# Performance work log

Measured on AMD Instinct MI355X. Metric: run time of the kernel, lower is better.

Reference implementation:

```python
import jax, jax.numpy as jnp
import numpy as np

B, S, D_IN, D_OUT = 4, 2048, 1024, 1024


def setup_inputs() -> dict:
    key = jax.random.key(0)
    k1, k2, k3, k4 = jax.random.split(key, 4)
    scale = 1.0 / np.sqrt(D_IN)
    return {
        "x": jax.random.normal(k1, (B, S, D_IN), dtype=jnp.float32),
        "W_q": jax.random.normal(k2, (D_IN, D_OUT), dtype=jnp.float32) * scale,
        "W_k": jax.random.normal(k3, (D_IN, D_OUT), dtype=jnp.float32) * scale,
        "W_v": jax.random.normal(k4, (D_IN, D_OUT), dtype=jnp.float32) * scale,
    }


def reference(x, W_q, W_k, W_v):
    # x: [B, S, D_IN]; weights stored as [D_IN, D_OUT] (transpose of torch Linear)
    q = x @ W_q  # [B, S, D_OUT]
    k = x @ W_k
    v = x @ W_v
    inv_sqrt_d = 1.0 / jnp.sqrt(jnp.asarray(k.shape[-1], dtype=q.dtype))
    scores = jnp.einsum("bqd,bkd->bqk", q, k) * inv_sqrt_d  # [B, S, S]
    n = x.shape[1]
    causal_mask = jnp.triu(jnp.ones((n, n), dtype=bool), k=1)  # True above diagonal
    scores = jnp.where(causal_mask, -jnp.inf, scores)
    attn = jax.nn.softmax(scores, axis=-1)  # dropout p=0.0 -> identity
    return jnp.einsum("bqk,bkd->bqd", attn, v)  # [B, S, D_OUT]
```

## Files before the change

kernel.cpp:

```cpp
#include <hip/hip_runtime.h>
#include <hip/hip_bf16.h>
#include <stdint.h>

typedef __bf16 bf16;
typedef bf16 bf16x8 __attribute__((ext_vector_type(8)));
typedef float f32x4 __attribute__((ext_vector_type(4)));

#define NB   4
#define SS   2048
#define DI   1024
#define DOUT 1024

__device__ __forceinline__ void gload_lds16(const void* g, void* l) {
  __builtin_amdgcn_global_load_lds(
      (const __attribute__((address_space(1))) void*)g,
      (__attribute__((address_space(3))) void*)l, 16, 0, 0);
}

#define BARX  { __builtin_amdgcn_s_barrier(); __builtin_amdgcn_sched_barrier(0); }
#define VMW12 asm volatile("s_waitcnt vmcnt(12)" ::: "memory")
#define VMW8  asm volatile("s_waitcnt vmcnt(8)"  ::: "memory")
#define VMW6  asm volatile("s_waitcnt vmcnt(6)"  ::: "memory")
#define VMW4  asm volatile("s_waitcnt vmcnt(4)"  ::: "memory")
#define VMW0  asm volatile("s_waitcnt vmcnt(0)"  ::: "memory")

__device__ __forceinline__ void r5_loop3(
    const bf16* __restrict__ Ag, int lda,
    const bf16* __restrict__ Bg, int ldb,
    int nt, char* lds, f32x4 (&acc)[8][4])
{
  const int tid = threadIdx.x, lane = tid & 63, w = tid >> 6;
  const int g    = (tid & 3) ^ ((tid >> 3) & 3);
  const int srow = tid >> 2;
  const int l15  = lane & 15, lg = lane >> 4;
  const int aoff = l15 * 64 + ((lg ^ ((l15 >> 1) & 3)) << 4);

  auto STG = [&](int t, int p) {
    char* Ab = lds + p * 24576;
    char* Bb = lds + p * 24576 + 8192;
#pragma unroll
    for (int i = 0; i < 2; ++i)
      gload_lds16(Ag + (size_t)(i * 64 + srow) * lda + t * 32 + g * 8,
                  Ab + i * 4096 + tid * 16);
#pragma unroll
    for (int i = 0; i < 4; ++i)
      gload_lds16(Bg + (size_t)(i * 64 + srow) * ldb + t * 32 + g * 8,
                  Bb + i * 4096 + tid * 16);
  };

  auto CMP = [&](int p) {
    const char* Ab = lds + p * 24576;
    const char* Bb = lds + p * 24576 + 8192 + w * 4096;
    bf16x8 a[8], bq[4];
#pragma unroll
    for (int am = 0; am < 8; ++am) a[am] = *(const bf16x8*)(Ab + am * 1024 + aoff);
#pragma unroll
    for (int fn = 0; fn < 4; ++fn) bq[fn] = *(const bf16x8*)(Bb + fn * 1024 + aoff);
    __builtin_amdgcn_s_setprio(1);
#pragma unroll
    for (int am = 0; am < 8; ++am)
#pragma unroll
      for (int fn = 0; fn < 4; ++fn)
        acc[am][fn] = __builtin_amdgcn_mfma_f32_16x16x32_bf16(
            a[am], bq[fn], acc[am][fn], 0, 0, 0);
    __builtin_amdgcn_s_setprio(0);
  };

  STG(0, 0);
  STG(1, 1);
  int pw = 2, pr = 0;
  for (int t = 0; t < nt - 2; ++t) {
    STG(t + 2, pw);
    VMW12;
    BARX;
    CMP(pr);
    BARX;
    pw = (pw == 2) ? 0 : pw + 1;
    pr = (pr == 2) ? 0 : pr + 1;
  }
  VMW6; BARX; CMP(pr); BARX;
  pr = (pr == 2) ? 0 : pr + 1;
  VMW0; BARX; CMP(pr);
}

__device__ __forceinline__ void r5h_loop3(
    const bf16* __restrict__ Ag, int lda,
    const bf16* __restrict__ Bg, int ldb,
    int nt, char* lds, f32x4 (&acc)[4][4])
{
  const int tid = threadIdx.x, lane = tid & 63, wid = tid >> 6;
  const int wr = wid >> 1, wc = wid & 1;
  const int g    = (tid & 3) ^ ((tid >> 3) & 3);
  const int srow = tid >> 2;
  const int l15  = lane & 15, lg = lane >> 4;
  const int aoff = l15 * 64 + ((lg ^ ((l15 >> 1) & 3)) << 4);

  auto STG = [&](int t, int p) {
    char* Ab = lds + p * 16384;
    char* Bb = lds + p * 16384 + 8192;
#pragma unroll
    for (int i = 0; i < 2; ++i) {
      gload_lds16(Ag + (size_t)(i * 64 + srow) * lda + t * 32 + g * 8,
                  Ab + i * 4096 + tid * 16);
      gload_lds16(Bg + (size_t)(i * 64 + srow) * ldb + t * 32 + g * 8,
                  Bb + i * 4096 + tid * 16);
    }
  };

  auto CMP = [&](int p) {
    const char* Ab = lds + p * 16384 + wr * 4096;
    const char* Bb = lds + p * 16384 + 8192 + wc * 4096;
    bf16x8 a[4], bq[4];
#pragma unroll
    for (int fm = 0; fm < 4; ++fm) a[fm] = *(const bf16x8*)(Ab + fm * 1024 + aoff);
#pragma unroll
    for (int fn = 0; fn < 4; ++fn) bq[fn] = *(const bf16x8*)(Bb + fn * 1024 + aoff);
    __builtin_amdgcn_s_setprio(1);
#pragma unroll
    for (int fm = 0; fm < 4; ++fm)
#pragma unroll
      for (int fn = 0; fn < 4; ++fn)
        acc[fm][fn] = __builtin_amdgcn_mfma_f32_16x16x32_bf16(
            a[fm], bq[fn], acc[fm][fn], 0, 0, 0);
    __builtin_amdgcn_s_setprio(0);
  };

  STG(0, 0);
  STG(1, 1);
  int pw = 2, pr = 0;
  for (int t = 0; t < nt - 2; ++t) {
    STG(t + 2, pw);
    VMW8;
    BARX;
    CMP(pr);
    BARX;
    pw = (pw == 2) ? 0 : pw + 1;
    pr = (pr == 2) ? 0 : pr + 1;
  }
  VMW4; BARX; CMP(pr); BARX;
  pr = (pr == 2) ? 0 : pr + 1;
  VMW0; BARX; CMP(pr);
}

__device__ __forceinline__ void acc_zero4(f32x4 (&acc)[4][4]) {
#pragma unroll
  for (int i = 0; i < 4; ++i)
#pragma unroll
    for (int j = 0; j < 4; ++j)
      acc[i][j] = (f32x4){0.f, 0.f, 0.f, 0.f};
}

__global__ __launch_bounds__(256) void k_cast_wt(const float* __restrict__ Wq,
                                                 const float* __restrict__ Wk,
                                                 const float* __restrict__ Wv,
                                                 bf16* __restrict__ WSq,
                                                 bf16* __restrict__ WSk,
                                                 bf16* __restrict__ WTv) {
  __shared__ float t[32][33];
  const int w = blockIdx.z;
  const int k0 = blockIdx.y * 32, c0 = blockIdx.x * 32;
  const int tx = threadIdx.x, ty = threadIdx.y;
  if (w < 2) {
    const float* W = w ? Wk : Wq;
    bf16* WS = w ? WSk : WSq;
#pragma unroll
    for (int i = 0; i < 4; ++i) {
      const size_t idx = (size_t)(k0 + ty + 8 * i) * DI + c0 + tx;
      WS[idx] = (bf16)W[idx];
    }
  } else {
#pragma unroll
    for (int i = 0; i < 4; ++i)
      t[ty + 8 * i][tx] = Wv[(size_t)(k0 + ty + 8 * i) * DI + c0 + tx];
    __syncthreads();
#pragma unroll
    for (int i = 0; i < 4; ++i)
      WTv[(size_t)(c0 + ty + 8 * i) * DI + k0 + tx] = (bf16)t[tx][ty + 8 * i];
  }
}

__global__ __launch_bounds__(256) void k_castx_mt(const float* __restrict__ x,
                                                  bf16* __restrict__ xb,
                                                  const bf16* __restrict__ WSk,
                                                  const bf16* __restrict__ WSq,
                                                  bf16* __restrict__ MT) {
  __shared__ __align__(16) char lds[49152];
  const int bid = blockIdx.x;
  if (bid < 64) {
    const int m0 = (bid >> 3) * 128, n0 = (bid & 7) * 128;
    f32x4 acc[4][4];
    acc_zero4(acc);
    r5h_loop3(WSk + (size_t)m0 * 1024, 1024, WSq + (size_t)n0 * 1024, 1024,
              32, lds, acc);
    const int lane = threadIdx.x & 63, wid = threadIdx.x >> 6;
    const int wr = wid >> 1, wc = wid & 1;
    const int r4 = (lane >> 4) * 4, cn = lane & 15;
#pragma unroll
    for (int fm = 0; fm < 4; ++fm)
#pragma unroll
      for (int fn = 0; fn < 4; ++fn) {
        const int row = m0 + wr * 64 + fm * 16 + r4;
        const int col = n0 + wc * 64 + fn * 16 + cn;
#pragma unroll
        for (int rr = 0; rr < 4; ++rr)
          MT[(size_t)(row + rr) * 1024 + col] = (bf16)acc[fm][fn][rr];
      }
  } else {
    const size_t i = ((size_t)(bid - 64) * 256 + threadIdx.x) * 8;
    const float4 a = *(const float4*)(x + i);
    const float4 c = *(const float4*)(x + i + 4);
    bf16x8 v;
    v[0] = (bf16)a.x; v[1] = (bf16)a.y; v[2] = (bf16)a.z; v[3] = (bf16)a.w;
    v[4] = (bf16)c.x; v[5] = (bf16)c.y; v[6] = (bf16)c.z; v[7] = (bf16)c.w;
    *(bf16x8*)(xb + i) = v;
  }
}

__global__ __launch_bounds__(256, 2) void k_tv(const bf16* __restrict__ X,
                                               const bf16* __restrict__ MT,
                                               const bf16* __restrict__ WTv,
                                               bf16* __restrict__ T,
                                               bf16* __restrict__ VT) {
  __shared__ __align__(16) char lds[73728];
  const int bid  = blockIdx.x;
  const int wgid = (bid & 7) * 64 + (bid >> 3);
  const int m0 = (wgid >> 3) * 128;
  const int n0 = (wgid & 7) * 256;

  const bf16* Bg = (n0 < 1024) ? MT + (size_t)n0 * 1024
                               : WTv + (size_t)(n0 - 1024) * 1024;

  f32x4 acc[8][4];
#pragma unroll
  for (int i = 0; i < 8; ++i)
#pragma unroll
    for (int j = 0; j < 4; ++j)
      acc[i][j] = (f32x4){0.f, 0.f, 0.f, 0.f};

  r5_loop3(X + (size_t)m0 * 1024, 1024, Bg, 1024, 32, lds, acc);

  const int lane = threadIdx.x & 63, w = threadIdx.x >> 6;
  const int r4 = (lane >> 4) * 4;
  const int cn = lane & 15;
  if (n0 < 1024) {
#pragma unroll
    for (int am = 0; am < 8; ++am) {
      const int row = m0 + am * 16 + r4;
#pragma unroll
      for (int fn = 0; fn < 4; ++fn) {
        const int n = n0 + w * 64 + fn * 16 + cn;
        const size_t base = (size_t)row * 1024 + n;
#pragma unroll
        for (int r = 0; r < 4; ++r)
          T[base + (size_t)r * 1024] = (bf16)acc[am][fn][r];
      }
    }
  } else {
    const int b_ = m0 >> 11;
    const int sb = m0 & 2047;
#pragma unroll
    for (int am = 0; am < 8; ++am)
#pragma unroll
      for (int fn = 0; fn < 4; ++fn) {
        const int d  = (n0 - 1024) + w * 64 + fn * 16 + cn;
        const int s0 = sb + am * 16 + r4;
        ushort4 pk;
        pk.x = __builtin_bit_cast(unsigned short, (bf16)acc[am][fn][0]);
        pk.y = __builtin_bit_cast(unsigned short, (bf16)acc[am][fn][1]);
        pk.z = __builtin_bit_cast(unsigned short, (bf16)acc[am][fn][2]);
        pk.w = __builtin_bit_cast(unsigned short, (bf16)acc[am][fn][3]);
        *(ushort4*)(VT + ((size_t)b_ * DOUT + d) * SS + s0) = pk;
      }
  }
}

__global__ __launch_bounds__(256, 3) void k_gemm_qk(const bf16* __restrict__ T,
                                                    const bf16* __restrict__ XB,
                                                    bf16* __restrict__ E,
                                                    float* __restrict__ RS) {
  __shared__ __align__(16) char lds[49152];
  const int wfl = blockIdx.x;
  const int b = wfl / 136;
  int r = wfl % 136;
  int i = 0;
  for (;;) { const int cnt = i + 1; if (r < cnt) break; r -= cnt; ++i; }
  const int m0 = i * 128, n0 = r * 128;

  f32x4 acc[4][4];
  acc_zero4(acc);
  r5h_loop3(T  + ((size_t)b * SS + m0) * 1024, 1024,
            XB + ((size_t)b * SS + n0) * 1024, 1024, 32, lds, acc);

  bf16* Eb = E + (size_t)b * SS * SS;
  float* RSb = RS + (size_t)b * SS;
  const float scale = 0.03125f;
  const int lane = threadIdx.x & 63, wid = threadIdx.x >> 6;
  const int wr = wid >> 1, wc = wid & 1;
  const int r4 = (lane >> 4) * 4, cn = lane & 15;

  float rsum[4][4];
#pragma unroll
  for (int fm = 0; fm < 4; ++fm)
#pragma unroll
    for (int rr = 0; rr < 4; ++rr) rsum[fm][rr] = 0.f;

#pragma unroll
  for (int fm = 0; fm < 4; ++fm)
#pragma unroll
    for (int fn = 0; fn < 4; ++fn) {
      const int n = n0 + wc * 64 + fn * 16 + cn;
      const int rowb = m0 + wr * 64 + fm * 16 + r4;
      const size_t bofs = (size_t)rowb * SS + n;
#pragma unroll
      for (int rr = 0; rr < 4; ++rr) {
        const float e = (n <= rowb + rr) ? __expf(acc[fm][fn][rr] * scale) : 0.f;
        Eb[bofs + (size_t)rr * SS] = (bf16)e;
        rsum[fm][rr] += e;
      }
    }

#pragma unroll
  for (int fm = 0; fm < 4; ++fm)
#pragma unroll
    for (int rr = 0; rr < 4; ++rr) {
      float s = rsum[fm][rr];
      s += __shfl_xor(s, 1);
      s += __shfl_xor(s, 2);
      s += __shfl_xor(s, 4);
      s += __shfl_xor(s, 8);
      if (cn == 0)
        atomicAdd(&RSb[m0 + wr * 64 + fm * 16 + r4 + rr], s);
    }
}

__global__ __launch_bounds__(256, 3) void k_gemm_pv(const bf16* __restrict__ P,
                                                    const bf16* __restrict__ VT,
                                                    const float* __restrict__ RS,
                                                    float* __restrict__ Out) {
  __shared__ __align__(16) char lds[49152];
  const int wfl = blockIdx.x;
  const int h = wfl >> 8;
  const int r = wfl & 255;
  const int b = r >> 6;
  const int t = r & 63;
  const int ip = t >> 3;
  const int j = t & 7;
  const int i = h ? (15 - ip) : ip;
  const int m0 = i * 128, n0 = j * 128;
  const int nt = 4 * (i + 1);

  f32x4 acc[4][4];
  acc_zero4(acc);
  r5h_loop3(P  + (size_t)b * SS * SS   + (size_t)m0 * SS, SS,
            VT + (size_t)b * DOUT * SS + (size_t)n0 * SS, SS,
            nt, lds, acc);

  float* Ob = Out + (size_t)b * SS * DOUT;
  const float* RSb = RS + (size_t)b * SS;
  const int lane = threadIdx.x & 63, wid = threadIdx.x >> 6;
  const int wr = wid >> 1, wc = wid & 1;
  const int r4 = (lane >> 4) * 4, cn = lane & 15;
#pragma unroll
  for (int fm = 0; fm < 4; ++fm) {
    const int rowb = m0 + wr * 64 + fm * 16 + r4;
    const float4 rs4 = *(const float4*)(RSb + rowb);
    float inv[4];
    inv[0] = 1.0f / rs4.x; inv[1] = 1.0f / rs4.y;
    inv[2] = 1.0f / rs4.z; inv[3] = 1.0f / rs4.w;
#pragma unroll
    for (int fn = 0; fn < 4; ++fn) {
      const int n = n0 + wc * 64 + fn * 16 + cn;
      const size_t bofs = (size_t)rowb * DOUT + n;
#pragma unroll
      for (int rr = 0; rr < 4; ++rr)
        Ob[bofs + (size_t)rr * DOUT] = acc[fm][fn][rr] * inv[rr];
    }
  }
}

extern "C" void kernel_launch(void* const* d_in, const int* in_sizes, int n_in,
                              void* d_out, int out_size, void* d_ws, size_t ws_size,
                              hipStream_t stream) {
  const float* x  = (const float*)d_in[0];
  const float* Wq = (const float*)d_in[1];
  const float* Wk = (const float*)d_in[2];
  const float* Wv = (const float*)d_in[3];
  float* out = (float*)d_out;
  char* ws = (char*)d_ws;

  bf16*  T   = (bf16*)(ws);
  bf16*  VT  = (bf16*)(ws + ((size_t)16 << 20));
  bf16*  E   = (bf16*)(ws + ((size_t)32 << 20));
  bf16*  XB  = (bf16*)(ws + ((size_t)64 << 20));
  bf16*  WSq = (bf16*)(ws + ((size_t)80 << 20));
  bf16*  WSk = (bf16*)(ws + ((size_t)82 << 20));
  bf16*  WTv = (bf16*)(ws + ((size_t)84 << 20));
  bf16*  MT  = (bf16*)(ws + ((size_t)86 << 20));
  float* RS  = (float*)(ws + ((size_t)88 << 20));

  hipMemsetAsync(RS, 0, (size_t)NB * SS * sizeof(float), stream);
  k_cast_wt<<<dim3(32, 32, 3), dim3(32, 8), 0, stream>>>(Wq, Wk, Wv, WSq, WSk, WTv);
  k_castx_mt<<<4160, 256, 0, stream>>>(x, XB, WSk, WSq, MT);
  k_tv<<<512, 256, 0, stream>>>(XB, MT, WTv, T, VT);
  k_gemm_qk<<<544, 256, 0, stream>>>(T, XB, E, RS);
  k_gemm_pv<<<512, 256, 0, stream>>>(E, VT, RS, out);
}
```

Baseline: 144.2 us.

## Split-K the Wk·Wqᵀ product with fp32 atomics and fuse weight casts

The 1024x1024 Wk·Wq^T product was computed by only 64 blocks over the full K. It is now split eight ways along K into 512 blocks that read the fp32 weights directly, convert them to bf16 in LDS, and atomically add their partials into an fp32 buffer. A separate small kernel then converts that buffer to bf16. This removes the separate bf16 weight-cast pass for Wq/Wk and exposes more parallelism on a stage that was latency bound. The cost is atomic traffic, a larger memset (which also zeroes RS through the contiguous layout), one extra launch, and a simpler unpipelined inner loop.

```diff
diff --git a/kernel.cpp b/kernel.cpp
--- a/kernel.cpp
+++ b/kernel.cpp
@@ -23,6 +23,13 @@
 #define VMW6  asm volatile("s_waitcnt vmcnt(6)"  ::: "memory")
 #define VMW4  asm volatile("s_waitcnt vmcnt(4)"  ::: "memory")
 #define VMW0  asm volatile("s_waitcnt vmcnt(0)"  ::: "memory")
+
+__device__ __forceinline__ bf16x8 cvt8(float4 a, float4 b) {
+  bf16x8 v;
+  v[0] = (bf16)a.x; v[1] = (bf16)a.y; v[2] = (bf16)a.z; v[3] = (bf16)a.w;
+  v[4] = (bf16)b.x; v[5] = (bf16)b.y; v[6] = (bf16)b.z; v[7] = (bf16)b.w;
+  return v;
+}
 
 __device__ __forceinline__ void r5_loop3(
     const bf16* __restrict__ Ag, int lda,
@@ -150,25 +157,81 @@
       acc[i][j] = (f32x4){0.f, 0.f, 0.f, 0.f};
 }
 
-__global__ __launch_bounds__(256) void k_cast_wt(const float* __restrict__ Wq,
-                                                 const float* __restrict__ Wk,
-                                                 const float* __restrict__ Wv,
-                                                 bf16* __restrict__ WSq,
-                                                 bf16* __restrict__ WSk,
-                                                 bf16* __restrict__ WTv) {
-  __shared__ float t[32][33];
-  const int w = blockIdx.z;
-  const int k0 = blockIdx.y * 32, c0 = blockIdx.x * 32;
-  const int tx = threadIdx.x, ty = threadIdx.y;
-  if (w < 2) {
-    const float* W = w ? Wk : Wq;
-    bf16* WS = w ? WSk : WSq;
-#pragma unroll
-    for (int i = 0; i < 4; ++i) {
-      const size_t idx = (size_t)(k0 + ty + 8 * i) * DI + c0 + tx;
-      WS[idx] = (bf16)W[idx];
-    }
+__global__ __launch_bounds__(256) void k_prep1(const float* __restrict__ x,
+                                               bf16* __restrict__ xb,
+                                               const float* __restrict__ Wq,
+                                               const float* __restrict__ Wk,
+                                               const float* __restrict__ Wv,
+                                               bf16* __restrict__ WTv,
+                                               float* __restrict__ MTf) {
+  __shared__ __align__(16) char lds[16384];
+  const int bid = blockIdx.x;
+  const int tid = threadIdx.x;
+
+  if (bid < 512) {
+    const int tile = bid >> 3, s = bid & 7;
+    const int m0 = (tile >> 3) * 128, n0 = (tile & 7) * 128;
+    const int k0 = s * 128;
+    const int lane = tid & 63, wid = tid >> 6;
+    const int wr = wid >> 1, wc = wid & 1;
+    const int g    = (tid & 3) ^ ((tid >> 3) & 3);
+    const int srow = tid >> 2;
+    const int l15  = lane & 15, lg = lane >> 4;
+    const int aoff = l15 * 64 + ((lg ^ ((l15 >> 1) & 3)) << 4);
+
+    f32x4 acc[4][4];
+    acc_zero4(acc);
+
+    for (int t = 0; t < 4; ++t) {
+#pragma unroll
+      for (int i = 0; i < 2; ++i) {
+        const float* ap = Wk + (size_t)(m0 + i * 64 + srow) * DI + k0 + t * 32 + g * 8;
+        const float* bp = Wq + (size_t)(n0 + i * 64 + srow) * DI + k0 + t * 32 + g * 8;
+        const float4 a0 = *(const float4*)ap, a1 = *(const float4*)(ap + 4);
+        const float4 b0 = *(const float4*)bp, b1 = *(const float4*)(bp + 4);
+        *(bf16x8*)(lds + i * 4096 + tid * 16)        = cvt8(a0, a1);
+        *(bf16x8*)(lds + 8192 + i * 4096 + tid * 16) = cvt8(b0, b1);
+      }
+      __syncthreads();
+      {
+        const char* Ab = lds + wr * 4096;
+        const char* Bb = lds + 8192 + wc * 4096;
+        bf16x8 a[4], bq[4];
+#pragma unroll
+        for (int fm = 0; fm < 4; ++fm) a[fm] = *(const bf16x8*)(Ab + fm * 1024 + aoff);
+#pragma unroll
+        for (int fn = 0; fn < 4; ++fn) bq[fn] = *(const bf16x8*)(Bb + fn * 1024 + aoff);
+#pragma unroll
+        for (int fm = 0; fm < 4; ++fm)
+#pragma unroll
+          for (int fn = 0; fn < 4; ++fn)
+            acc[fm][fn] = __builtin_amdgcn_mfma_f32_16x16x32_bf16(
+                a[fm], bq[fn], acc[fm][fn], 0, 0, 0);
+      }
+      __syncthreads();
+    }
+
+    const int r4 = (lane >> 4) * 4, cn = lane & 15;
+#pragma unroll
+    for (int fm = 0; fm < 4; ++fm)
+#pragma unroll
+      for (int fn = 0; fn < 4; ++fn) {
+        const int rowb = m0 + wr * 64 + fm * 16 + r4;
+        const int col  = n0 + wc * 64 + fn * 16 + cn;
+#pragma unroll
+        for (int rr = 0; rr < 4; ++rr)
+          atomicAdd(&MTf[(size_t)(rowb + rr) * 1024 + col], acc[fm][fn][rr]);
+      }
+  } else if (bid < 4608) {
+    const size_t i = ((size_t)(bid - 512) * 256 + tid) * 8;
+    const float4 a = *(const float4*)(x + i);
+    const float4 c = *(const float4*)(x + i + 4);
+    *(bf16x8*)(xb + i) = cvt8(a, c);
   } else {
+    float (*t)[33] = (float (*)[33])lds;
+    const int tt = bid - 4608;
+    const int c0 = (tt & 31) * 32, k0 = (tt >> 5) * 32;
+    const int tx = tid & 31, ty = tid >> 5;
 #pragma unroll
     for (int i = 0; i < 4; ++i)
       t[ty + 8 * i][tx] = Wv[(size_t)(k0 + ty + 8 * i) * DI + c0 + tx];
@@ -179,41 +242,12 @@
   }
 }
 
-__global__ __launch_bounds__(256) void k_castx_mt(const float* __restrict__ x,
-                                                  bf16* __restrict__ xb,
-                                                  const bf16* __restrict__ WSk,
-                                                  const bf16* __restrict__ WSq,
-                                                  bf16* __restrict__ MT) {
-  __shared__ __align__(16) char lds[49152];
-  const int bid = blockIdx.x;
-  if (bid < 64) {
-    const int m0 = (bid >> 3) * 128, n0 = (bid & 7) * 128;
-    f32x4 acc[4][4];
-    acc_zero4(acc);
-    r5h_loop3(WSk + (size_t)m0 * 1024, 1024, WSq + (size_t)n0 * 1024, 1024,
-              32, lds, acc);
-    const int lane = threadIdx.x & 63, wid = threadIdx.x >> 6;
-    const int wr = wid >> 1, wc = wid & 1;
-    const int r4 = (lane >> 4) * 4, cn = lane & 15;
-#pragma unroll
-    for (int fm = 0; fm < 4; ++fm)
-#pragma unroll
-      for (int fn = 0; fn < 4; ++fn) {
-        const int row = m0 + wr * 64 + fm * 16 + r4;
-        const int col = n0 + wc * 64 + fn * 16 + cn;
-#pragma unroll
-        for (int rr = 0; rr < 4; ++rr)
-          MT[(size_t)(row + rr) * 1024 + col] = (bf16)acc[fm][fn][rr];
-      }
-  } else {
-    const size_t i = ((size_t)(bid - 64) * 256 + threadIdx.x) * 8;
-    const float4 a = *(const float4*)(x + i);
-    const float4 c = *(const float4*)(x + i + 4);
-    bf16x8 v;
-    v[0] = (bf16)a.x; v[1] = (bf16)a.y; v[2] = (bf16)a.z; v[3] = (bf16)a.w;
-    v[4] = (bf16)c.x; v[5] = (bf16)c.y; v[6] = (bf16)c.z; v[7] = (bf16)c.w;
-    *(bf16x8*)(xb + i) = v;
-  }
+__global__ __launch_bounds__(256) void k_prep2(const float* __restrict__ MTf,
+                                               bf16* __restrict__ MT) {
+  const size_t i = ((size_t)blockIdx.x * 256 + threadIdx.x) * 8;
+  const float4 a = *(const float4*)(MTf + i);
+  const float4 c = *(const float4*)(MTf + i + 4);
+  *(bf16x8*)(MT + i) = cvt8(a, c);
 }
 
 __global__ __launch_bounds__(256, 2) void k_tv(const bf16* __restrict__ X,
@@ -392,15 +426,14 @@
   bf16*  VT  = (bf16*)(ws + ((size_t)16 << 20));
   bf16*  E   = (bf16*)(ws + ((size_t)32 << 20));
   bf16*  XB  = (bf16*)(ws + ((size_t)64 << 20));
-  bf16*  WSq = (bf16*)(ws + ((size_t)80 << 20));
-  bf16*  WSk = (bf16*)(ws + ((size_t)82 << 20));
-  bf16*  WTv = (bf16*)(ws + ((size_t)84 << 20));
-  bf16*  MT  = (bf16*)(ws + ((size_t)86 << 20));
+  bf16*  WTv = (bf16*)(ws + ((size_t)80 << 20));
+  bf16*  MT  = (bf16*)(ws + ((size_t)82 << 20));
+  float* MTf = (float*)(ws + ((size_t)84 << 20));
   float* RS  = (float*)(ws + ((size_t)88 << 20));
 
-  hipMemsetAsync(RS, 0, (size_t)NB * SS * sizeof(float), stream);
-  k_cast_wt<<<dim3(32, 32, 3), dim3(32, 8), 0, stream>>>(Wq, Wk, Wv, WSq, WSk, WTv);
-  k_castx_mt<<<4160, 256, 0, stream>>>(x, XB, WSk, WSq, MT);
+  hipMemsetAsync(MTf, 0, ((size_t)4 << 20) + (size_t)NB * SS * sizeof(float), stream);
+  k_prep1<<<5632, 256, 0, stream>>>(x, XB, Wq, Wk, Wv, WTv, MTf);
+  k_prep2<<<512, 256, 0, stream>>>(MTf, MT);
   k_tv<<<512, 256, 0, stream>>>(XB, MT, WTv, T, VT);
   k_gemm_qk<<<544, 256, 0, stream>>>(T, XB, E, RS);
   k_gemm_pv<<<512, 256, 0, stream>>>(E, VT, RS, out);
```

After: 162.2 us. 12.5% more time.
